# Kernel tuning notes

Measured on AMD Instinct MI355X. Metric: run time of the kernel, lower is better.

The kernel has to match this reference:

```python
import jax, jax.numpy as jnp
import numpy as np

EPS = 1e-5

def _batchnorm(h, gamma, beta):
    # training-mode BatchNorm1d over node dim, biased variance
    mu = jnp.mean(h, axis=0)
    var = jnp.mean((h - mu) ** 2, axis=0)
    return (h - mu) * jax.lax.rsqrt(var + EPS) * gamma + beta

def _sage(x, src, dst, n, Wl, b, Wr):
    # sum-aggregate source features into destinations, then linear + root linear
    agg = jax.ops.segment_sum(x[src], dst, num_segments=n)  # [N, F]
    return agg @ Wl + b + x @ Wr

def setup_inputs() -> dict:
    key = jax.random.key(0)
    ks = jax.random.split(key, 8)
    N, E, F, H, O = 200000, 1200000, 64, 128, 128
    s = lambda fan_in: 1.0 / np.sqrt(fan_in)
    return {
        "x": jax.random.normal(ks[0], (N, F), jnp.float32),
        "edge_index": jax.random.randint(ks[1], (2, E), 0, N, jnp.int64),
        "W1l": jax.random.normal(ks[2], (F, H), jnp.float32) * s(F),
        "b1": jnp.zeros((H,), jnp.float32),
        "W1r": jax.random.normal(ks[3], (F, H), jnp.float32) * s(F),
        "g1": jnp.ones((H,), jnp.float32),
        "be1": jnp.zeros((H,), jnp.float32),
        "W2l": jax.random.normal(ks[4], (H, O), jnp.float32) * s(H),
        "b2": jnp.zeros((O,), jnp.float32),
        "W2r": jax.random.normal(ks[5], (H, O), jnp.float32) * s(H),
        "g2": jnp.ones((O,), jnp.float32),
        "be2": jnp.zeros((O,), jnp.float32),
    }

def reference(x, edge_index, W1l, b1, W1r, g1, be1, W2l, b2, W2r, g2, be2):
    n = x.shape[0]
    src, dst = edge_index[0], edge_index[1]
    h = jax.nn.relu(_sage(x, src, dst, n, W1l, b1, W1r))
    h = _batchnorm(h, g1, be1)
    h = jax.nn.relu(_sage(h, src, dst, n, W2l, b2, W2r))
    h = _batchnorm(h, g2, be2)
    return jax.nn.relu(h)
```

## Files before the change

### kernel.cpp

```cpp
#include <hip/hip_runtime.h>

#define N_NODES 200000
#define N_EDGES 1200000
#define F_IN    64
#define F_H     128
#define BN_EPS  1e-5f

typedef short bf16x8 __attribute__((ext_vector_type(8)));
typedef float f32x4  __attribute__((ext_vector_type(4)));
typedef unsigned short us4 __attribute__((ext_vector_type(4)));

__device__ __forceinline__ unsigned short f2bf(float f) {
    union { float f; unsigned u; } v; v.f = f;
    unsigned r = (v.u + 0x7FFFu + ((v.u >> 16) & 1u)) >> 16;
    return (unsigned short)r;
}
__device__ __forceinline__ float bf2f(unsigned short b) {
    union { unsigned u; float f; } v; v.u = ((unsigned)b) << 16;
    return v.f;
}

__global__ void pack_weights_kernel(const float* __restrict__ W,
                                    const float* __restrict__ kscale,
                                    short* __restrict__ P, int KT)
{
    int t = blockIdx.x * 256 + threadIdx.x;
    if (t >= 8 * KT * 64) return;
    int lane = t & 63;
    int kt   = (t >> 6) % KT;
    int nt   = t / (64 * KT);
    int k0   = kt * 32 + (lane >> 4) * 8;
    int n    = nt * 16 + (lane & 15);
#pragma unroll
    for (int j = 0; j < 8; ++j) {
        float w = W[(size_t)(k0 + j) * 128 + n];
        if (kscale) w *= kscale[k0 + j];
        P[(size_t)t * 8 + j] = (short)f2bf(w);
    }
}

__global__ __launch_bounds__(256) void hist_kernel(const int* __restrict__ ei,
                                                   int* __restrict__ deg, int E)
{
    int e = blockIdx.x * 256 + threadIdx.x;
    if (e < E) atomicAdd(&deg[ei[E + e]], 1);
}

__global__ __launch_bounds__(256) void scan1_kernel(const int* __restrict__ deg,
        int* __restrict__ part, int* __restrict__ bsum, int n)
{
    __shared__ int s[256];
    int t = threadIdx.x;
    int base = blockIdx.x * 1024 + t * 4;
    int v[4];
#pragma unroll
    for (int j = 0; j < 4; ++j) v[j] = (base + j < n) ? deg[base + j] : 0;
    int tsum = v[0] + v[1] + v[2] + v[3];
    s[t] = tsum;
    __syncthreads();
    for (int off = 1; off < 256; off <<= 1) {
        int xv = (t >= off) ? s[t - off] : 0;
        __syncthreads();
        s[t] += xv;
        __syncthreads();
    }
    int excl = s[t] - tsum;
#pragma unroll
    for (int j = 0; j < 4; ++j) {
        if (base + j < n) part[base + j] = excl;
        excl += v[j];
    }
    if (t == 255) bsum[blockIdx.x] = s[255];
}

__global__ void scan2_kernel(int* __restrict__ bsum, int nb)
{
    __shared__ int s[256];
    int t = threadIdx.x;
    int v = (t < nb) ? bsum[t] : 0;
    s[t] = v;
    __syncthreads();
    for (int off = 1; off < 256; off <<= 1) {
        int xv = (t >= off) ? s[t - off] : 0;
        __syncthreads();
        s[t] += xv;
        __syncthreads();
    }
    if (t < nb) bsum[t] = s[t] - v;
}

__global__ __launch_bounds__(256) void scan3_kernel(
    const int* __restrict__ part, const int* __restrict__ bsum,
    const int* __restrict__ deg, int* __restrict__ rowptr,
    int* __restrict__ cursor, float* __restrict__ degf, int n, int E)
{
    int i = blockIdx.x * 256 + threadIdx.x;
    if (i == 0) rowptr[n] = E;
    if (i >= n) return;
    int r = part[i] + bsum[i >> 10];
    rowptr[i] = r;
    cursor[i] = r;
    degf[i]   = (float)deg[i];
}

__global__ __launch_bounds__(256) void fill_kernel(const int* __restrict__ ei,
        int* __restrict__ cursor, int* __restrict__ ssrc, int E)
{
    int e = blockIdx.x * 256 + threadIdx.x;
    if (e >= E) return;
    int d = ei[E + e];
    int pos = atomicAdd(&cursor[d], 1);
    ssrc[pos] = ei[e];
}

__global__ __launch_bounds__(256) void gather1_kernel(
    const float* __restrict__ x, const int* __restrict__ rowptr,
    const int* __restrict__ ssrc, unsigned short* __restrict__ aggb)
{
    const int tid  = threadIdx.x;
    const int wv   = tid >> 6;
    const int lane = tid & 63;
    const int sub  = lane >> 4;
    const int li   = lane & 15;
    const int row  = blockIdx.x * 16 + wv * 4 + sub;

    int b = rowptr[row], e = rowptr[row + 1];
    float4 acc = {0.f, 0.f, 0.f, 0.f};
    if (b < e) {
        int s = ssrc[b];
        for (int j = b; j < e; ++j) {
            int sn = (j + 1 < e) ? ssrc[j + 1] : 0;
            float4 v = ((const float4*)(x + (size_t)s * F_IN))[li];
            acc.x += v.x; acc.y += v.y; acc.z += v.z; acc.w += v.w;
            s = sn;
        }
    }
    us4 o;
    o.x = f2bf(acc.x); o.y = f2bf(acc.y); o.z = f2bf(acc.z); o.w = f2bf(acc.w);
    *(us4*)(aggb + (size_t)row * F_IN + li * 4) = o;
}

__global__ __launch_bounds__(256) void gather2_kernel(
    const unsigned short* __restrict__ t1, const int* __restrict__ rowptr,
    const int* __restrict__ ssrc, unsigned short* __restrict__ aggb)
{
    const int tid  = threadIdx.x;
    const int wv   = tid >> 6;
    const int lane = tid & 63;
    const int sub  = lane >> 4;
    const int li   = lane & 15;
    const int row  = blockIdx.x * 16 + wv * 4 + sub;

    int b = rowptr[row], e = rowptr[row + 1];
    float acc[8] = {};
    if (b < e) {
        int s = ssrc[b];
        for (int j = b; j < e; ++j) {
            int sn = (j + 1 < e) ? ssrc[j + 1] : 0;
            bf16x8 v = *(const bf16x8*)(t1 + (size_t)s * F_H + li * 8);
#pragma unroll
            for (int k = 0; k < 8; ++k) acc[k] += bf2f((unsigned short)v[k]);
            s = sn;
        }
    }
    bf16x8 o;
#pragma unroll
    for (int k = 0; k < 8; ++k) o[k] = (short)f2bf(acc[k]);
    *(bf16x8*)(aggb + (size_t)row * F_H + li * 8) = o;
}

template<int K, bool L2>
__global__ __launch_bounds__(256) void gemm_mfma_kernel(
    const unsigned short* __restrict__ Ab,
    const float* __restrict__ Xf,
    const unsigned short* __restrict__ Xb,
    const short* __restrict__ Wlp, const short* __restrict__ Wrp,
    const float* __restrict__ bias,
    const float* __restrict__ c2, const float* __restrict__ degf,
    float* __restrict__ outF, unsigned short* __restrict__ outB,
    float* __restrict__ gsum, float* __restrict__ gsq, int nTiles)
{
    constexpr int KT = K / 32;
    constexpr int CH = K * 16;
    __shared__ bf16x8 wlds[2 * CH];
    __shared__ float sS[128];
    __shared__ float sQ[128];

    const int tid  = threadIdx.x;
    const int lane = tid & 63;
    const int wv   = tid >> 6;
    const int m    = lane & 15;
    const int quad = lane >> 4;
    const int col_l = m;

    {
        const bf16x8* s1 = (const bf16x8*)Wlp;
        const bf16x8* s2 = (const bf16x8*)Wrp;
        for (int i = tid; i < CH; i += 256) wlds[i] = s1[i];
        for (int i = tid; i < CH; i += 256) wlds[CH + i] = s2[i];
    }
    if (tid < 128) { sS[tid] = 0.f; sQ[tid] = 0.f; }
    __syncthreads();

    float bcol[8], ccol[8];
#pragma unroll
    for (int nt = 0; nt < 8; ++nt) {
        bcol[nt] = bias[nt * 16 + col_l];
        if constexpr (L2) ccol[nt] = c2[nt * 16 + col_l];
    }

    float stS[8] = {}, stQ[8] = {};

    for (int tile = blockIdx.x; tile < nTiles; tile += gridDim.x) {
        const int rowbase = tile * 256 + wv * 64;
        f32x4 acc[4][8] = {};

#pragma unroll
        for (int kt = 0; kt < KT; ++kt) {
            const int k0 = kt * 32 + quad * 8;
            bf16x8 af[4], xf[4];
#pragma unroll
            for (int st = 0; st < 4; ++st) {
                int r  = rowbase + st * 16 + m;
                int rc = r < N_NODES ? r : N_NODES - 1;
                af[st] = *(const bf16x8*)(Ab + (size_t)rc * K + k0);
                if constexpr (L2) {
                    xf[st] = *(const bf16x8*)(Xb + (size_t)rc * K + k0);
                } else {
                    const float4* xp = (const float4*)(Xf + (size_t)rc * K + k0);
                    float4 x0 = xp[0], x1 = xp[1];
                    xf[st][0] = (short)f2bf(x0.x); xf[st][1] = (short)f2bf(x0.y);
                    xf[st][2] = (short)f2bf(x0.z); xf[st][3] = (short)f2bf(x0.w);
                    xf[st][4] = (short)f2bf(x1.x); xf[st][5] = (short)f2bf(x1.y);
                    xf[st][6] = (short)f2bf(x1.z); xf[st][7] = (short)f2bf(x1.w);
                }
            }
#pragma unroll
            for (int nt = 0; nt < 8; ++nt) {
                bf16x8 wl = wlds[(nt * KT + kt) * 64 + lane];
#pragma unroll
                for (int st = 0; st < 4; ++st)
                    acc[st][nt] = __builtin_amdgcn_mfma_f32_16x16x32_bf16(
                        af[st], wl, acc[st][nt], 0, 0, 0);
                bf16x8 wr = wlds[CH + (nt * KT + kt) * 64 + lane];
#pragma unroll
                for (int st = 0; st < 4; ++st)
                    acc[st][nt] = __builtin_amdgcn_mfma_f32_16x16x32_bf16(
                        xf[st], wr, acc[st][nt], 0, 0, 0);
            }
        }

#pragma unroll
        for (int st = 0; st < 4; ++st) {
            const int orow = rowbase + st * 16 + quad * 4;
            float dg[4];
            if constexpr (L2) {
#pragma unroll
                for (int r = 0; r < 4; ++r) {
                    int rr = orow + r;
                    dg[r] = (rr < N_NODES) ? degf[rr] : 0.f;
                }
            }
#pragma unroll
            for (int nt = 0; nt < 8; ++nt) {
                int col = nt * 16 + col_l;
#pragma unroll
                for (int r = 0; r < 4; ++r) {
                    int rr = orow + r;
                    if (rr < N_NODES) {
                        float base = L2 ? fmaf(dg[r], ccol[nt], bcol[nt]) : bcol[nt];
                        float v = fmaxf(acc[st][nt][r] + base, 0.f);
                        if constexpr (L2) outF[(size_t)rr * 128 + col] = v;
                        else              outB[(size_t)rr * 128 + col] = f2bf(v);
                        stS[nt] += v;
                        stQ[nt] = fmaf(v, v, stQ[nt]);
                    }
                }
            }
        }
    }

#pragma unroll
    for (int nt = 0; nt < 8; ++nt) {
        atomicAdd(&sS[nt * 16 + col_l], stS[nt]);
        atomicAdd(&sQ[nt * 16 + col_l], stQ[nt]);
    }
    __syncthreads();
    if (tid < 128) {
        atomicAdd(&gsum[tid], sS[tid]);
        atomicAdd(&gsq[tid],  sQ[tid]);
    }
}

__global__ void bn_finalize_kernel(
    const float* __restrict__ gsum, const float* __restrict__ gsq,
    const float* __restrict__ g, const float* __restrict__ be,
    float* __restrict__ scale, float* __restrict__ shift, float invN)
{
    int c = threadIdx.x;
    float mean = gsum[c] * invN;
    float var  = fmaxf(gsq[c] * invN - mean * mean, 0.f);
    float sc   = g[c] * rsqrtf(var + BN_EPS);
    scale[c] = sc;
    shift[c] = be[c] - mean * sc;
}

__global__ void bn_fold_kernel(
    const float* __restrict__ shift1, const float* __restrict__ W2l,
    const float* __restrict__ W2r, const float* __restrict__ b2,
    float* __restrict__ c2, float* __restrict__ crb)
{
    int col = threadIdx.x;
    float a = 0.f, r = 0.f;
    for (int k = 0; k < 128; ++k) {
        float s = shift1[k];
        a = fmaf(s, W2l[(size_t)k * 128 + col], a);
        r = fmaf(s, W2r[(size_t)k * 128 + col], r);
    }
    c2[col]  = a;
    crb[col] = r + b2[col];
}

__global__ __launch_bounds__(256) void bn_apply_relu_kernel(
    float* __restrict__ h, const float* __restrict__ scale,
    const float* __restrict__ shift, int n4)
{
    int i = blockIdx.x * 256 + threadIdx.x;
    if (i >= n4) return;
    int cb = i & 31;
    float4 v  = ((float4*)h)[i];
    float4 sc = ((const float4*)scale)[cb];
    float4 sh = ((const float4*)shift)[cb];
    v.x = fmaxf(fmaf(v.x, sc.x, sh.x), 0.f);
    v.y = fmaxf(fmaf(v.y, sc.y, sh.y), 0.f);
    v.z = fmaxf(fmaf(v.z, sc.z, sh.z), 0.f);
    v.w = fmaxf(fmaf(v.w, sc.w, sh.w), 0.f);
    ((float4*)h)[i] = v;
}

extern "C" void kernel_launch(void* const* d_in, const int* in_sizes, int n_in,
                              void* d_out, int out_size, void* d_ws, size_t ws_size,
                              hipStream_t stream) {
    const float* x   = (const float*)d_in[0];
    const int*   ei  = (const int*)d_in[1];
    const float* W1l = (const float*)d_in[2];
    const float* b1  = (const float*)d_in[3];
    const float* W1r = (const float*)d_in[4];
    const float* g1  = (const float*)d_in[5];
    const float* be1 = (const float*)d_in[6];
    const float* W2l = (const float*)d_in[7];
    const float* b2  = (const float*)d_in[8];
    const float* W2r = (const float*)d_in[9];
    const float* g2  = (const float*)d_in[10];
    const float* be2 = (const float*)d_in[11];
    float* out = (float*)d_out;

    const int N = N_NODES, E = N_EDGES;
    const int NB1 = (N + 1023) / 1024;
    const int nTiles = (N + 255) / 256;

    float* ws     = (float*)d_ws;
    float* gsum1  = ws;        float* gsq1   = ws + 128;
    float* gsum2  = ws + 256;  float* gsq2   = ws + 384;
    float* scale1 = ws + 512;  float* shift1 = ws + 640;
    float* scale2 = ws + 768;  float* shift2 = ws + 896;
    float* c2v    = ws + 1024; float* crb    = ws + 1152;
    short* W1lp = (short*)(ws + 1536);
    short* W1rp = (short*)(ws + 1536 + 4096);
    short* W2lp = (short*)(ws + 1536 + 8192);
    short* W2rp = (short*)(ws + 1536 + 16384);
    int*   deg    = (int*)(ws + 26112);
    int*   part   = deg + N;
    int*   bsum   = part + N;
    int*   rowptr = bsum + 1024;
    int*   cursor = rowptr + (N + 1024);
    float* degf   = (float*)(cursor + N);
    int*   ssrc   = (int*)(degf + N);
    unsigned short* t1   = (unsigned short*)(ssrc + E);
    unsigned short* aggb = t1 + (size_t)N * F_H;

    hipMemsetAsync(ws, 0, 1024 * sizeof(float), stream);
    hipMemsetAsync(deg, 0, (size_t)N * sizeof(int), stream);
    pack_weights_kernel<<<4, 256, 0, stream>>>(W1l, nullptr, W1lp, 2);
    pack_weights_kernel<<<4, 256, 0, stream>>>(W1r, nullptr, W1rp, 2);
    hist_kernel<<<(E + 255) / 256, 256, 0, stream>>>(ei, deg, E);
    scan1_kernel<<<NB1, 256, 0, stream>>>(deg, part, bsum, N);
    scan2_kernel<<<1, 256, 0, stream>>>(bsum, NB1);
    scan3_kernel<<<(N + 255) / 256, 256, 0, stream>>>(part, bsum, deg, rowptr,
                                                      cursor, degf, N, E);
    fill_kernel<<<(E + 255) / 256, 256, 0, stream>>>(ei, cursor, ssrc, E);

    gather1_kernel<<<N / 16, 256, 0, stream>>>(x, rowptr, ssrc, aggb);
    gemm_mfma_kernel<F_IN, false><<<512, 256, 0, stream>>>(
        aggb, x, nullptr, W1lp, W1rp, b1, nullptr, nullptr,
        nullptr, t1, gsum1, gsq1, nTiles);
    bn_finalize_kernel<<<1, 128, 0, stream>>>(gsum1, gsq1, g1, be1,
                                              scale1, shift1, 1.f / N);

    pack_weights_kernel<<<8, 256, 0, stream>>>(W2l, scale1, W2lp, 4);
    pack_weights_kernel<<<8, 256, 0, stream>>>(W2r, scale1, W2rp, 4);
    bn_fold_kernel<<<1, 128, 0, stream>>>(shift1, W2l, W2r, b2, c2v, crb);
    gather2_kernel<<<N / 16, 256, 0, stream>>>(t1, rowptr, ssrc, aggb);
    gemm_mfma_kernel<F_H, true><<<512, 256, 0, stream>>>(
        aggb, nullptr, t1, W2lp, W2rp, crb, c2v, degf,
        out, nullptr, gsum2, gsq2, nTiles);
    bn_finalize_kernel<<<1, 128, 0, stream>>>(gsum2, gsq2, g2, be2,
                                              scale2, shift2, 1.f / N);
    bn_apply_relu_kernel<<<(N * F_H / 4 + 255) / 256, 256, 0, stream>>>(
        out, scale2, shift2, N * F_H / 4);
}
```

Baseline: 632.9 us.

## Launch one GEMM block per tile, read weights from global, spread BN atomics

The fused SAGE GEMM kernels drop the grid-stride persistent loop over 512 blocks and launch one block per 256-row tile. The packed weights are no longer staged into LDS; each wave reads its weight fragments straight from global memory, relying on L1/L2 caching. The BN sum and sum-of-squares atomics are split across 4 replicated slots chosen by block index to cut contention, and the finalize kernel sums the 4 slots. The trade-off is more blocks, each issuing more global weight loads and more global atomics in total, in exchange for less LDS use and higher occupancy.

Result: slower. 660.1 us (+4.3%).

```diff
diff --git a/kernel.cpp b/kernel.cpp
--- a/kernel.cpp
+++ b/kernel.cpp
@@ -174,15 +174,13 @@
     const unsigned short* __restrict__ Ab,
     const float* __restrict__ Xf,
     const unsigned short* __restrict__ Xb,
-    const short* __restrict__ Wlp, const short* __restrict__ Wrp,
+    const bf16x8* __restrict__ Wlp, const bf16x8* __restrict__ Wrp,
     const float* __restrict__ bias,
     const float* __restrict__ c2, const float* __restrict__ degf,
     float* __restrict__ outF, unsigned short* __restrict__ outB,
-    float* __restrict__ gsum, float* __restrict__ gsq, int nTiles)
+    float* __restrict__ gsum, float* __restrict__ gsq)
 {
     constexpr int KT = K / 32;
-    constexpr int CH = K * 16;
-    __shared__ bf16x8 wlds[2 * CH];
     __shared__ float sS[128];
     __shared__ float sQ[128];
 
@@ -191,104 +189,96 @@
     const int wv   = tid >> 6;
     const int m    = lane & 15;
     const int quad = lane >> 4;
-    const int col_l = m;
-
-    {
-        const bf16x8* s1 = (const bf16x8*)Wlp;
-        const bf16x8* s2 = (const bf16x8*)Wrp;
-        for (int i = tid; i < CH; i += 256) wlds[i] = s1[i];
-        for (int i = tid; i < CH; i += 256) wlds[CH + i] = s2[i];
-    }
+    const int rowbase = blockIdx.x * 256 + wv * 64;
+
     if (tid < 128) { sS[tid] = 0.f; sQ[tid] = 0.f; }
+
+    float bcol[8], ccol[8];
+#pragma unroll
+    for (int nt = 0; nt < 8; ++nt) {
+        bcol[nt] = bias[nt * 16 + m];
+        if constexpr (L2) ccol[nt] = c2[nt * 16 + m];
+    }
+
+    f32x4 acc[4][8] = {};
+
+#pragma unroll
+    for (int kt = 0; kt < KT; ++kt) {
+        const int k0 = kt * 32 + quad * 8;
+        bf16x8 af[4], xf[4];
+#pragma unroll
+        for (int st = 0; st < 4; ++st) {
+            int r  = rowbase + st * 16 + m;
+            int rc = r < N_NODES ? r : N_NODES - 1;
+            af[st] = *(const bf16x8*)(Ab + (size_t)rc * K + k0);
+            if constexpr (L2) {
+                xf[st] = *(const bf16x8*)(Xb + (size_t)rc * K + k0);
+            } else {
+                const float4* xp = (const float4*)(Xf + (size_t)rc * K + k0);
+                float4 x0 = xp[0], x1 = xp[1];
+                xf[st][0] = (short)f2bf(x0.x); xf[st][1] = (short)f2bf(x0.y);
+                xf[st][2] = (short)f2bf(x0.z); xf[st][3] = (short)f2bf(x0.w);
+                xf[st][4] = (short)f2bf(x1.x); xf[st][5] = (short)f2bf(x1.y);
+                xf[st][6] = (short)f2bf(x1.z); xf[st][7] = (short)f2bf(x1.w);
+            }
+        }
+#pragma unroll
+        for (int nt = 0; nt < 8; ++nt) {
+            bf16x8 wl = Wlp[(nt * KT + kt) * 64 + lane];
+#pragma unroll
+            for (int st = 0; st < 4; ++st)
+                acc[st][nt] = __builtin_amdgcn_mfma_f32_16x16x32_bf16(
+                    af[st], wl, acc[st][nt], 0, 0, 0);
+            bf16x8 wr = Wrp[(nt * KT + kt) * 64 + lane];
+#pragma unroll
+            for (int st = 0; st < 4; ++st)
+                acc[st][nt] = __builtin_amdgcn_mfma_f32_16x16x32_bf16(
+                    xf[st], wr, acc[st][nt], 0, 0, 0);
+        }
+    }
+
     __syncthreads();
 
-    float bcol[8], ccol[8];
-#pragma unroll
-    for (int nt = 0; nt < 8; ++nt) {
-        bcol[nt] = bias[nt * 16 + col_l];
-        if constexpr (L2) ccol[nt] = c2[nt * 16 + col_l];
-    }
-
     float stS[8] = {}, stQ[8] = {};
-
-    for (int tile = blockIdx.x; tile < nTiles; tile += gridDim.x) {
-        const int rowbase = tile * 256 + wv * 64;
-        f32x4 acc[4][8] = {};
-
-#pragma unroll
-        for (int kt = 0; kt < KT; ++kt) {
-            const int k0 = kt * 32 + quad * 8;
-            bf16x8 af[4], xf[4];
-#pragma unroll
-            for (int st = 0; st < 4; ++st) {
-                int r  = rowbase + st * 16 + m;
-                int rc = r < N_NODES ? r : N_NODES - 1;
-                af[st] = *(const bf16x8*)(Ab + (size_t)rc * K + k0);
-                if constexpr (L2) {
-                    xf[st] = *(const bf16x8*)(Xb + (size_t)rc * K + k0);
-                } else {
-                    const float4* xp = (const float4*)(Xf + (size_t)rc * K + k0);
-                    float4 x0 = xp[0], x1 = xp[1];
-                    xf[st][0] = (short)f2bf(x0.x); xf[st][1] = (short)f2bf(x0.y);
-                    xf[st][2] = (short)f2bf(x0.z); xf[st][3] = (short)f2bf(x0.w);
-                    xf[st][4] = (short)f2bf(x1.x); xf[st][5] = (short)f2bf(x1.y);
-                    xf[st][6] = (short)f2bf(x1.z); xf[st][7] = (short)f2bf(x1.w);
+#pragma unroll
+    for (int st = 0; st < 4; ++st) {
+        const int orow = rowbase + st * 16 + quad * 4;
+        float dg[4];
+        if constexpr (L2) {
+#pragma unroll
+            for (int r = 0; r < 4; ++r) {
+                int rr = orow + r;
+                dg[r] = (rr < N_NODES) ? degf[rr] : 0.f;
+            }
+        }
+#pragma unroll
+        for (int nt = 0; nt < 8; ++nt) {
+            int col = nt * 16 + m;
+#pragma unroll
+            for (int r = 0; r < 4; ++r) {
+                int rr = orow + r;
+                if (rr < N_NODES) {
+                    float base = L2 ? fmaf(dg[r], ccol[nt], bcol[nt]) : bcol[nt];
+                    float v = fmaxf(acc[st][nt][r] + base, 0.f);
+                    if constexpr (L2) outF[(size_t)rr * 128 + col] = v;
+                    else              outB[(size_t)rr * 128 + col] = f2bf(v);
+                    stS[nt] += v;
+                    stQ[nt] = fmaf(v, v, stQ[nt]);
                 }
             }
-#pragma unroll
-            for (int nt = 0; nt < 8; ++nt) {
-                bf16x8 wl = wlds[(nt * KT + kt) * 64 + lane];
-#pragma unroll
-                for (int st = 0; st < 4; ++st)
-                    acc[st][nt] = __builtin_amdgcn_mfma_f32_16x16x32_bf16(
-                        af[st], wl, acc[st][nt], 0, 0, 0);
-                bf16x8 wr = wlds[CH + (nt * KT + kt) * 64 + lane];
-#pragma unroll
-                for (int st = 0; st < 4; ++st)
-                    acc[st][nt] = __builtin_amdgcn_mfma_f32_16x16x32_bf16(
-                        xf[st], wr, acc[st][nt], 0, 0, 0);
-            }
-        }
-
-#pragma unroll
-        for (int st = 0; st < 4; ++st) {
-            const int orow = rowbase + st * 16 + quad * 4;
-            float dg[4];
-            if constexpr (L2) {
-#pragma unroll
-                for (int r = 0; r < 4; ++r) {
-                    int rr = orow + r;
-                    dg[r] = (rr < N_NODES) ? degf[rr] : 0.f;
-                }
-            }
-#pragma unroll
-            for (int nt = 0; nt < 8; ++nt) {
-                int col = nt * 16 + col_l;
-#pragma unroll
-                for (int r = 0; r < 4; ++r) {
-                    int rr = orow + r;
-                    if (rr < N_NODES) {
-                        float base = L2 ? fmaf(dg[r], ccol[nt], bcol[nt]) : bcol[nt];
-                        float v = fmaxf(acc[st][nt][r] + base, 0.f);
-                        if constexpr (L2) outF[(size_t)rr * 128 + col] = v;
-                        else              outB[(size_t)rr * 128 + col] = f2bf(v);
-                        stS[nt] += v;
-                        stQ[nt] = fmaf(v, v, stQ[nt]);
-                    }
-                }
-            }
         }
     }
 
 #pragma unroll
     for (int nt = 0; nt < 8; ++nt) {
-        atomicAdd(&sS[nt * 16 + col_l], stS[nt]);
-        atomicAdd(&sQ[nt * 16 + col_l], stQ[nt]);
+        atomicAdd(&sS[nt * 16 + m], stS[nt]);
+        atomicAdd(&sQ[nt * 16 + m], stQ[nt]);
     }
     __syncthreads();
+    const int rep = (blockIdx.x & 3) * 128;
     if (tid < 128) {
-        atomicAdd(&gsum[tid], sS[tid]);
-        atomicAdd(&gsq[tid],  sQ[tid]);
+        atomicAdd(&gsum[rep + tid], sS[tid]);
+        atomicAdd(&gsq[rep + tid],  sQ[tid]);
     }
 }
 
@@ -298,8 +288,10 @@
     float* __restrict__ scale, float* __restrict__ shift, float invN)
 {
     int c = threadIdx.x;
-    float mean = gsum[c] * invN;
-    float var  = fmaxf(gsq[c] * invN - mean * mean, 0.f);
+    float s = gsum[c] + gsum[128 + c] + gsum[256 + c] + gsum[384 + c];
+    float q = gsq[c]  + gsq[128 + c]  + gsq[256 + c]  + gsq[384 + c];
+    float mean = s * invN;
+    float var  = fmaxf(q * invN - mean * mean, 0.f);
     float sc   = g[c] * rsqrtf(var + BN_EPS);
     scale[c] = sc;
     shift[c] = be[c] - mean * sc;
@@ -357,19 +349,19 @@
 
     const int N = N_NODES, E = N_EDGES;
     const int NB1 = (N + 1023) / 1024;
-    const int nTiles = (N + 255) / 256;
+    const int nT  = (N + 255) / 256;
 
     float* ws     = (float*)d_ws;
-    float* gsum1  = ws;        float* gsq1   = ws + 128;
-    float* gsum2  = ws + 256;  float* gsq2   = ws + 384;
-    float* scale1 = ws + 512;  float* shift1 = ws + 640;
-    float* scale2 = ws + 768;  float* shift2 = ws + 896;
-    float* c2v    = ws + 1024; float* crb    = ws + 1152;
-    short* W1lp = (short*)(ws + 1536);
-    short* W1rp = (short*)(ws + 1536 + 4096);
-    short* W2lp = (short*)(ws + 1536 + 8192);
-    short* W2rp = (short*)(ws + 1536 + 16384);
-    int*   deg    = (int*)(ws + 26112);
+    float* gsum1  = ws;          float* gsq1   = ws + 512;
+    float* gsum2  = ws + 1024;   float* gsq2   = ws + 1536;
+    float* scale1 = ws + 2048;   float* shift1 = ws + 2176;
+    float* scale2 = ws + 2304;   float* shift2 = ws + 2432;
+    float* c2v    = ws + 2560;   float* crb    = ws + 2688;
+    short* W1lp = (short*)(ws + 3072);
+    short* W1rp = (short*)(ws + 3072 + 4096);
+    short* W2lp = (short*)(ws + 3072 + 8192);
+    short* W2rp = (short*)(ws + 3072 + 16384);
+    int*   deg    = (int*)(ws + 27648);
     int*   part   = deg + N;
     int*   bsum   = part + N;
     int*   rowptr = bsum + 1024;
@@ -379,7 +371,7 @@
     unsigned short* t1   = (unsigned short*)(ssrc + E);
     unsigned short* aggb = t1 + (size_t)N * F_H;
 
-    hipMemsetAsync(ws, 0, 1024 * sizeof(float), stream);
+    hipMemsetAsync(ws, 0, 2048 * sizeof(float), stream);
     hipMemsetAsync(deg, 0, (size_t)N * sizeof(int), stream);
     pack_weights_kernel<<<4, 256, 0, stream>>>(W1l, nullptr, W1lp, 2);
     pack_weights_kernel<<<4, 256, 0, stream>>>(W1r, nullptr, W1rp, 2);
@@ -391,9 +383,9 @@
     fill_kernel<<<(E + 255) / 256, 256, 0, stream>>>(ei, cursor, ssrc, E);
 
     gather1_kernel<<<N / 16, 256, 0, stream>>>(x, rowptr, ssrc, aggb);
-    gemm_mfma_kernel<F_IN, false><<<512, 256, 0, stream>>>(
-        aggb, x, nullptr, W1lp, W1rp, b1, nullptr, nullptr,
-        nullptr, t1, gsum1, gsq1, nTiles);
+    gemm_mfma_kernel<F_IN, false><<<nT, 256, 0, stream>>>(
+        aggb, x, nullptr, (const bf16x8*)W1lp, (const bf16x8*)W1rp, b1,
+        nullptr, nullptr, nullptr, t1, gsum1, gsq1);
     bn_finalize_kernel<<<1, 128, 0, stream>>>(gsum1, gsq1, g1, be1,
                                               scale1, shift1, 1.f / N);
 
@@ -401,9 +393,9 @@
     pack_weights_kernel<<<8, 256, 0, stream>>>(W2r, scale1, W2rp, 4);
     bn_fold_kernel<<<1, 128, 0, stream>>>(shift1, W2l, W2r, b2, c2v, crb);
     gather2_kernel<<<N / 16, 256, 0, stream>>>(t1, rowptr, ssrc, aggb);
-    gemm_mfma_kernel<F_H, true><<<512, 256, 0, stream>>>(
-        aggb, nullptr, t1, W2lp, W2rp, crb, c2v, degf,
-        out, nullptr, gsum2, gsq2, nTiles);
+    gemm_mfma_kernel<F_H, true><<<nT, 256, 0, stream>>>(
+        aggb, nullptr, t1, (const bf16x8*)W2lp, (const bf16x8*)W2rp, crb,
+        c2v, degf, out, nullptr, gsum2, gsq2);
     bn_finalize_kernel<<<1, 128, 0, stream>>>(gsum2, gsq2, g2, be2,
                                               scale2, shift2, 1.f / N);
     bn_apply_relu_kernel<<<(N * F_H / 4 + 255) / 256, 256, 0, stream>>>(
```
